# Performance work log

Measured on AMD Instinct MI355X. Metric: run time of the kernel, lower is better.

## Reference

```python
import jax, jax.numpy as jnp
import numpy as np

B, S, D, H = 4, 2048, 512, 16
HD = D // H          # head_dim = 32
ROPE_DIM = HD        # rope_pct = 1.0
NEG = -1e30


def apply_rope(x):
    # x: [B, H, S, HD]; rotate first ROPE_DIM dims, half-split (NeoX) convention
    half = ROPE_DIM // 2
    pos = jnp.arange(S, dtype=jnp.float32)
    inv_freq = 1.0 / (10000.0 ** (jnp.arange(0, ROPE_DIM, 2, dtype=jnp.float32) / ROPE_DIM))
    ang = pos[:, None] * inv_freq[None, :]          # [S, half]
    cos, sin = jnp.cos(ang), jnp.sin(ang)           # broadcast over B,H
    x1 = x[..., :half]
    x2 = x[..., half:ROPE_DIM]
    r1 = x1 * cos - x2 * sin
    r2 = x2 * cos + x1 * sin
    rest = x[..., ROPE_DIM:]
    return jnp.concatenate([r1, r2, rest], axis=-1)


def setup_inputs() -> dict:
    key = jax.random.key(0)
    ks = jax.random.split(key, 7)
    x = jax.random.normal(ks[0], (B, S, D), dtype=jnp.float32)
    # causal mask: True = block (j > i)
    attn_mask = jnp.triu(jnp.ones((S, S), dtype=bool), k=1)
    # padding mask: True = PAD; random lengths in [S//2, S]
    lengths = jax.random.randint(ks[1], (B,), S // 2, S + 1)
    key_padding_mask = jnp.arange(S)[None, :] >= lengths[:, None]
    scale = D ** -0.5
    Wq = jax.random.normal(ks[2], (D, D), dtype=jnp.float32) * scale
    Wk = jax.random.normal(ks[3], (D, D), dtype=jnp.float32) * scale
    Wv = jax.random.normal(ks[4], (D, D), dtype=jnp.float32) * scale
    Wo = jax.random.normal(ks[5], (D, D), dtype=jnp.float32) * scale
    return {"x": x, "attn_mask": attn_mask, "key_padding_mask": key_padding_mask,
            "Wq": Wq, "Wk": Wk, "Wv": Wv, "Wo": Wo}


def reference(x, attn_mask, key_padding_mask, Wq, Wk, Wv, Wo):
    scale = HD ** -0.5
    # nn.Linear: y = x @ W.T
    q = (x @ Wq.T).reshape(B, S, H, HD).transpose(0, 2, 1, 3)  # [B,H,S,HD]
    k = (x @ Wk.T).reshape(B, S, H, HD).transpose(0, 2, 1, 3)
    v = (x @ Wv.T).reshape(B, S, H, HD).transpose(0, 2, 1, 3)
    q = apply_rope(q)
    k = apply_rope(k)
    scores = jnp.einsum('bhid,bhjd->bhij', q, k) * scale       # [B,H,S,S]
    scores = jnp.where(key_padding_mask[:, None, None, :], NEG, scores)
    scores = jnp.where(attn_mask[None, None, :, :], NEG, scores)
    probs = jax.nn.softmax(scores.astype(jnp.float32), axis=-1)
    probs = jnp.nan_to_num(probs, nan=0.0)
    ctx = jnp.einsum('bhij,bhjd->bhid', probs, v)              # [B,H,S,HD]
    ctx = ctx.transpose(0, 2, 1, 3).reshape(B, S, D)
    ctx = jnp.where(key_padding_mask[:, :, None], 0.0, ctx)
    return ctx @ Wo.T
```

## Files before the change

kernel.cpp:

```cpp
#include <hip/hip_runtime.h>
#include <hip/hip_bf16.h>

#define B_ 4
#define S_ 2048
#define D_ 512
#define H_ 16
#define HD_ 32

typedef __bf16 bf16;
typedef __bf16 bf16x4 __attribute__((ext_vector_type(4)));
typedef __bf16 bf16x8 __attribute__((ext_vector_type(8)));
typedef float f32x4 __attribute__((ext_vector_type(4)));

__device__ __forceinline__ f32x4 mfma16(bf16x8 a, bf16x8 b, f32x4 c) {
  return __builtin_amdgcn_mfma_f32_16x16x32_bf16(a, b, c, 0, 0, 0);
}

__device__ __forceinline__ void gload16(const bf16* g, bf16* l) {
  __builtin_amdgcn_global_load_lds(
      (const __attribute__((address_space(1))) void*)g,
      (__attribute__((address_space(3))) void*)l, 16, 0, 0);
}

__device__ __forceinline__ bf16x8 cvt8(const float* __restrict__ p) {
  const f32x4* v = (const f32x4*)p;
  f32x4 a = v[0], b = v[1];
  bf16x8 r;
  r[0] = (bf16)a[0]; r[1] = (bf16)a[1]; r[2] = (bf16)a[2]; r[3] = (bf16)a[3];
  r[4] = (bf16)b[0]; r[5] = (bf16)b[1]; r[6] = (bf16)b[2]; r[7] = (bf16)b[3];
  return r;
}

__device__ __forceinline__ bf16x8 pack8(f32x4 a, f32x4 b) {
  bf16x8 r;
  r[0] = (bf16)a[0]; r[1] = (bf16)a[1]; r[2] = (bf16)a[2]; r[3] = (bf16)a[3];
  r[4] = (bf16)b[0]; r[5] = (bf16)b[1]; r[6] = (bf16)b[2]; r[7] = (bf16)b[3];
  return r;
}

__global__ __launch_bounds__(256) void prep_kernel(
    const float* __restrict__ wq, const float* __restrict__ wk,
    const float* __restrict__ wv, const float* __restrict__ wo,
    const unsigned char* __restrict__ am, const unsigned char* __restrict__ kpm,
    bf16* __restrict__ dq, bf16* __restrict__ dk, bf16* __restrict__ dv,
    bf16* __restrict__ dwo, int* __restrict__ lengths_out,
    float* __restrict__ costab, float* __restrict__ sintab) {
  int bid = blockIdx.x;
  if (bid < 512) {
    int mat = bid >> 7;
    size_t i = (size_t)(bid & 127) * 256 + threadIdx.x;
    const float* s = (mat == 0) ? wq : (mat == 1) ? wk : (mat == 2) ? wv : wo;
    bf16* d = (mat == 0) ? dq : (mat == 1) ? dk : (mat == 2) ? dv : dwo;
    *(bf16x8*)(d + i * 8) = cvt8(s + i * 8);
  } else if (bid == 512) {
    int b = threadIdx.x >> 6, lane = threadIdx.x & 63;
    int esize;
    if (am[1] == 1) esize = 1;
    else if (am[2] == 0x80 && am[3] == 0x3F) esize = 2;
    else if (am[3] == 0x3C) esize = 2;
    else if (am[4] == 1) esize = 4;
    else if (am[6] == 0x80 && am[7] == 0x3F) esize = 4;
    else if (am[8] == 1) esize = 8;
    else esize = 1;
    int cnt = 0;
    for (int i = lane; i < S_; i += 64) {
      size_t off = ((size_t)b * S_ + i) * (size_t)esize;
      unsigned char nz = 0;
      for (int e = 0; e < esize; ++e) nz |= kpm[off + e];
      cnt += (nz == 0) ? 1 : 0;
    }
    for (int off = 1; off < 64; off <<= 1) cnt += __shfl_xor(cnt, off);
    if (lane == 0) lengths_out[b] = cnt;
  } else {
    int ti = (bid - 513) * 256 + threadIdx.x;
    int s = ti >> 4, cc = ti & 15;
    float invf = powf(10000.0f, -(float)cc * (1.0f / 16.0f));
    float ang = (float)s * invf;
    costab[ti] = cosf(ang);
    sintab[ti] = sinf(ang);
  }
}

__global__ __launch_bounds__(256) void qkv_rope_kernel(
    const float* __restrict__ x, const bf16* __restrict__ Wq,
    const bf16* __restrict__ Wk, const bf16* __restrict__ Wv,
    const float* __restrict__ costab, const float* __restrict__ sintab,
    bf16* __restrict__ q_ws, bf16* __restrict__ k_ws, bf16* __restrict__ vt_ws) {
  __shared__ __align__(16) bf16 smem[12288];
#define AS(b) (smem + (b) * 2048)
#define BS(b) (smem + 4096 + (b) * 4096)
#define CT smem

  int bid = (blockIdx.x & 7) * 192 + (blockIdx.x >> 3);
  int brow = bid / 12, bc = bid % 12;
  int mat = bc >> 2;
  const bf16* W = (mat == 0) ? Wq : (mat == 1) ? Wk : Wv;
  int row0 = brow * 64;
  int col0 = (bc & 3) * 128;

  int tid = threadIdx.x;
  int w = tid >> 6, l = tid & 63;
  int wr = w >> 1, wc = w & 1;
  int g = l >> 4, c = l & 15;
  int lrow = l >> 2;
  int lcol = (l & 3) * 8;
  int arow = tid >> 2;
  int acol = (tid & 3) * 8;

  f32x4 acc[2][4];
  f32x4 zero = {0.f, 0.f, 0.f, 0.f};
#pragma unroll
  for (int m = 0; m < 2; ++m)
#pragma unroll
    for (int n = 0; n < 4; ++n) acc[m][n] = zero;

  *(bf16x8*)(AS(0) + arow * 32 + acol) =
      cvt8(x + (size_t)(row0 + arow) * 512 + acol);
#pragma unroll
  for (int j = 0; j < 2; ++j) {
    int chunk = w * 2 + j;
    gload16(W + (size_t)(col0 + chunk * 16 + lrow) * 512 + lcol,
            BS(0) + chunk * 512);
  }
  __syncthreads();
  int cur = 0;

#pragma unroll 1
  for (int k0 = 0; k0 < 512; k0 += 32) {
    bool more = (k0 < 480);
    f32x4 a0, a1;
    if (more) {
      const f32x4* src =
          (const f32x4*)(x + (size_t)(row0 + arow) * 512 + k0 + 32 + acol);
      a0 = src[0];
      a1 = src[1];
#pragma unroll
      for (int j = 0; j < 2; ++j) {
        int chunk = w * 2 + j;
        gload16(W + (size_t)(col0 + chunk * 16 + lrow) * 512 + k0 + 32 + lcol,
                BS(cur ^ 1) + chunk * 512);
      }
    }
    bf16x8 af[2], bfr[4];
#pragma unroll
    for (int m = 0; m < 2; ++m)
      af[m] = *(const bf16x8*)(AS(cur) + (wr * 32 + m * 16 + c) * 32 + g * 8);
#pragma unroll
    for (int n = 0; n < 4; ++n)
      bfr[n] = *(const bf16x8*)(BS(cur) + (wc * 64 + n * 16 + c) * 32 + g * 8);
#pragma unroll
    for (int m = 0; m < 2; ++m)
#pragma unroll
      for (int n = 0; n < 4; ++n) acc[m][n] = mfma16(af[m], bfr[n], acc[m][n]);
    if (more) {
      *(bf16x8*)(AS(cur ^ 1) + arow * 32 + acol) = pack8(a0, a1);
      __syncthreads();
      cur ^= 1;
    }
  }

  if (mat < 2) {
    bf16* dst = (mat == 0) ? q_ws : k_ws;
    const float esc =
        (mat == 0) ? (0.17677669529663687f * 1.4426950408889634f) : 1.0f;
#pragma unroll
    for (int m = 0; m < 2; ++m) {
      int rbase = row0 + wr * 32 + m * 16 + g * 4;
#pragma unroll
      for (int r = 0; r < 4; ++r) {
        int grow = rbase + r;
        int bb = grow >> 11, s = grow & (S_ - 1);
        float cs = costab[s * 16 + c];
        float sn = sintab[s * 16 + c];
#pragma unroll
        for (int np = 0; np < 2; ++np) {
          int n = np * 2;
          int obase = col0 + wc * 64 + n * 16;
          int h = obase >> 5;
          float a0v = acc[m][n][r], a1v = acc[m][n + 1][r];
          size_t base = (((size_t)bb * H_ + h) * S_ + s) * HD_;
          dst[base + c] = (bf16)((a0v * cs - a1v * sn) * esc);
          dst[base + c + 16] = (bf16)((a1v * cs + a0v * sn) * esc);
        }
      }
    }
  } else {
    __syncthreads();
#pragma unroll
    for (int m = 0; m < 2; ++m) {
#pragma unroll
      for (int n = 0; n < 4; ++n) {
        int o = wc * 64 + n * 16 + c;
        int sb = wr * 32 + m * 16 + g * 4;
        bf16x4 q4;
        q4[0] = (bf16)acc[m][n][0]; q4[1] = (bf16)acc[m][n][1];
        q4[2] = (bf16)acc[m][n][2]; q4[3] = (bf16)acc[m][n][3];
        *(bf16x4*)(&CT[o * 72 + sb]) = q4;
      }
    }
    __syncthreads();
    int o_l = tid >> 1, sh = (tid & 1) * 32;
    int o = col0 + o_l;
    int h = o >> 5, hd = o & 31;
    int bb2 = row0 >> 11, sr = row0 & (S_ - 1);
    size_t dst = (((size_t)bb2 * H_ + h) * HD_ + hd) * S_ + sr + sh;
#pragma unroll
    for (int j = 0; j < 4; ++j)
      *(bf16x8*)(vt_ws + dst + j * 8) =
          *(const bf16x8*)(&CT[o_l * 72 + sh + j * 8]);
  }
#undef AS
#undef BS
#undef CT
}

__global__ __launch_bounds__(256) void attn_kernel(
    const bf16* __restrict__ q_ws, const bf16* __restrict__ k_ws,
    const bf16* __restrict__ vt_ws, const int* __restrict__ lengths,
    bf16* __restrict__ ctx_ws) {
  __shared__ __align__(16) bf16 Ks[2][4096];
  __shared__ __align__(16) bf16 Vts[2][4096];
  __shared__ __align__(16) bf16 Ps[4][1024];

  int id = blockIdx.x;
  int xcd = id & 7;
  int ix = id >> 3;
  int p = ix & 15;
  int bh = xcd + 8 * (ix >> 4);
  int bb = bh >> 4, h = bh & 15;
  int tid = threadIdx.x, w = tid >> 6, l = tid & 63, g = l >> 4, c = l & 15;
  const size_t bh_base = ((size_t)bb * H_ + h) * (size_t)S_ * HD_;
  int len = lengths[bb];
  int rowrel = w * 16 + c;

  int srowK = w * 16 + (l & 15), skgK = l >> 4;
  int srowV = w * 8 + (l & 7), ssgV = l >> 3;
  int slotK8 = (skgK * 16 + (srowK & 15) + ((srowK >> 4) << 6)) * 8;
  int slotV8 =
      ((ssgV & 3) * 16 + (srowV & 15) + (((ssgV >> 2) + ((srowV >> 4) << 1)) << 6)) * 8;

  bf16 one = (bf16)1.0f;
  bf16x8 onesf;
#pragma unroll
  for (int i = 0; i < 8; ++i) onesf[i] = one;

#pragma unroll 1
  for (int phase = 0; phase < 2; ++phase) {
    int qt = phase ? (31 - p) : p;
    int q0 = qt * 64 + w * 16;
    int T = qt + 1;

    bf16x8 qf = *(const bf16x8*)(q_ws + bh_base + (size_t)(q0 + c) * HD_ + g * 8);

    f32x4 zero = {0.f, 0.f, 0.f, 0.f};
    f32x4 ctxa[2];
    ctxa[0] = zero; ctxa[1] = zero;
    f32x4 lsum = zero;

    const bf16* kbase = k_ws + bh_base + (size_t)srowK * HD_ + skgK * 8;
    const bf16* vbase = vt_ws + bh_base + (size_t)srowV * S_ + ssgV * 8;

    bf16x8 rK0 = *(const bf16x8*)kbase;
    bf16x8 rV0 = *(const bf16x8*)vbase;
    bf16x8 rK1 = rK0, rV1 = rV0;
    if (T > 1) {
      rK1 = *(const bf16x8*)(kbase + 64 * HD_);
      rV1 = *(const bf16x8*)(vbase + 64);
    }
    __syncthreads();
    *(bf16x8*)(&Ks[0][slotK8]) = rK0;
    *(bf16x8*)(&Vts[0][slotV8]) = rV0;
    *(bf16x8*)(&Ks[0][2048 + slotK8]) = rK1;
    *(bf16x8*)(&Vts[0][2048 + slotV8]) = rV1;
    __syncthreads();
    int cur = 0;

    auto body = [&](int t, int off) {
      const bf16* KsC = &Ks[cur][off];
      const bf16* VtsC = &Vts[cur][off];
      f32x4 sacc[4];
#pragma unroll
      for (int n = 0; n < 4; ++n) {
        bf16x8 kf = *(const bf16x8*)(&KsC[(l + (n << 6)) * 8]);
        sacc[n] = mfma16(kf, qf, zero);
      }

      float sv[4][4];
      if (t != qt) {
#pragma unroll
        for (int n = 0; n < 4; ++n)
#pragma unroll
          for (int r = 0; r < 4; ++r)
            sv[n][r] = __builtin_amdgcn_exp2f(sacc[n][r]);
      } else {
#pragma unroll
        for (int n = 0; n < 4; ++n) {
          int jr = n * 16 + g * 4;
#pragma unroll
          for (int r = 0; r < 4; ++r) {
            float e = __builtin_amdgcn_exp2f(sacc[n][r]);
            sv[n][r] = (jr + r > rowrel) ? 0.f : e;
          }
        }
      }

#pragma unroll
      for (int n = 0; n < 4; ++n) {
        bf16x4 pk;
        pk[0] = (bf16)sv[n][0]; pk[1] = (bf16)sv[n][1];
        pk[2] = (bf16)sv[n][2]; pk[3] = (bf16)sv[n][3];
        int chunk = 2 * n + (g >> 1);
        int poff = ((chunk >> 2) << 9) + ((chunk & 3) * 16 + c) * 8 + ((g & 1) << 2);
        *(bf16x4*)(&Ps[w][poff]) = pk;
      }

      bf16x8 pf0 = *(const bf16x8*)(&Ps[w][l * 8]);
      bf16x8 pf1 = *(const bf16x8*)(&Ps[w][512 + l * 8]);

      lsum = mfma16(pf0, onesf, lsum);
      lsum = mfma16(pf1, onesf, lsum);

#pragma unroll
      for (int n2 = 0; n2 < 2; ++n2) {
        bf16x8 v0 = *(const bf16x8*)(&VtsC[(l + ((2 * n2) << 6)) * 8]);
        bf16x8 v1 = *(const bf16x8*)(&VtsC[(l + ((1 + 2 * n2) << 6)) * 8]);
        ctxa[n2] = mfma16(pf0, v0, ctxa[n2]);
        ctxa[n2] = mfma16(pf1, v1, ctxa[n2]);
      }
    };

#pragma unroll 1
    for (int r = 0;; ++r) {
      int t0 = 2 * r, t1 = 2 * r + 1;
      bool more = (t0 + 2 < T);
      if (more) {
        const bf16* kp = kbase + (size_t)(t0 + 2) * 64 * HD_;
        const bf16* vp = vbase + (t0 + 2) * 64;
        rK0 = *(const bf16x8*)kp;
        rV0 = *(const bf16x8*)vp;
        rK1 = *(const bf16x8*)(kp + 64 * HD_);
        rV1 = *(const bf16x8*)(vp + 64);
      }
      body(t0, 0);
      if (t1 < T) body(t1, 2048);
      if (!more) break;
      *(bf16x8*)(&Ks[cur ^ 1][slotK8]) = rK0;
      *(bf16x8*)(&Vts[cur ^ 1][slotV8]) = rV0;
      *(bf16x8*)(&Ks[cur ^ 1][2048 + slotK8]) = rK1;
      *(bf16x8*)(&Vts[cur ^ 1][2048 + slotV8]) = rV1;
      __syncthreads();
      cur ^= 1;
    }

#pragma unroll
    for (int n = 0; n < 2; ++n)
#pragma unroll
      for (int r = 0; r < 4; ++r) {
        int qr = q0 + g * 4 + r;
        float val = ctxa[n][r] / lsum[r];
        if (qr >= len) val = 0.f;
        ctx_ws[(((size_t)bb * S_ + qr) * H_ + h) * HD_ + n * 16 + c] = (bf16)val;
      }
  }
}

__global__ __launch_bounds__(256) void out_proj_kernel(
    const bf16* __restrict__ ctx, const bf16* __restrict__ Wo,
    float* __restrict__ out) {
  __shared__ __align__(16) bf16 As[2][2048];
  __shared__ __align__(16) bf16 Bs[2][4096];

  int bid = (blockIdx.x & 7) * 64 + (blockIdx.x >> 3);
  int brow = bid >> 2, bc = bid & 3;
  int row0 = brow * 64, col0 = bc * 128;
  int tid = threadIdx.x;
  int w = tid >> 6, l = tid & 63;
  int wr = w >> 1, wc = w & 1;
  int g = l >> 4, c = l & 15;
  int lrow = l >> 2;
  int lcol = (l & 3) * 8;

  f32x4 acc[2][4];
  f32x4 zero = {0.f, 0.f, 0.f, 0.f};
#pragma unroll
  for (int m = 0; m < 2; ++m)
#pragma unroll
    for (int n = 0; n < 4; ++n) acc[m][n] = zero;

#pragma unroll
  for (int j = 0; j < 3; ++j) {
    int chunk = w * 3 + j;
    if (chunk < 4)
      gload16(ctx + (size_t)(row0 + chunk * 16 + lrow) * 512 + lcol,
              As[0] + chunk * 512);
    else
      gload16(Wo + (size_t)(col0 + (chunk - 4) * 16 + lrow) * 512 + lcol,
              Bs[0] + (chunk - 4) * 512);
  }
  __syncthreads();
  int cur = 0;

#pragma unroll 1
  for (int k0 = 0; k0 < 512; k0 += 32) {
    bool more = (k0 < 480);
    if (more) {
#pragma unroll
      for (int j = 0; j < 3; ++j) {
        int chunk = w * 3 + j;
        if (chunk < 4)
          gload16(ctx + (size_t)(row0 + chunk * 16 + lrow) * 512 + k0 + 32 + lcol,
                  As[cur ^ 1] + chunk * 512);
        else
          gload16(Wo + (size_t)(col0 + (chunk - 4) * 16 + lrow) * 512 + k0 + 32 +
                      lcol,
                  Bs[cur ^ 1] + (chunk - 4) * 512);
      }
    }
    bf16x8 af[2], bfr[4];
#pragma unroll
    for (int m = 0; m < 2; ++m)
      af[m] = *(const bf16x8*)(As[cur] + (wr * 32 + m * 16 + c) * 32 + g * 8);
#pragma unroll
    for (int n = 0; n < 4; ++n)
      bfr[n] = *(const bf16x8*)(Bs[cur] + (wc * 64 + n * 16 + c) * 32 + g * 8);
#pragma unroll
    for (int m = 0; m < 2; ++m)
#pragma unroll
      for (int n = 0; n < 4; ++n) acc[m][n] = mfma16(af[m], bfr[n], acc[m][n]);
    if (more) {
      __syncthreads();
      cur ^= 1;
    }
  }

#pragma unroll
  for (int m = 0; m < 2; ++m) {
    int rbase = row0 + wr * 32 + m * 16 + g * 4;
#pragma unroll
    for (int n = 0; n < 4; ++n) {
      int o = col0 + wc * 64 + n * 16 + c;
#pragma unroll
      for (int r = 0; r < 4; ++r)
        out[(size_t)(rbase + r) * 512 + o] = acc[m][n][r];
    }
  }
}

extern "C" void kernel_launch(void* const* d_in, const int* in_sizes, int n_in,
                              void* d_out, int out_size, void* d_ws,
                              size_t ws_size, hipStream_t stream) {
  const float* x = (const float*)d_in[0];
  const unsigned char* am = (const unsigned char*)d_in[1];
  const unsigned char* kpm = (const unsigned char*)d_in[2];
  const float* Wq = (const float*)d_in[3];
  const float* Wk = (const float*)d_in[4];
  const float* Wv = (const float*)d_in[5];
  const float* Wo = (const float*)d_in[6];
  float* out = (float*)d_out;

  char* ws = (char*)d_ws;
  int* lengths = (int*)ws;
  const size_t QKV_ELEMS = (size_t)B_ * H_ * S_ * HD_;
  const size_t W_ELEMS = (size_t)D_ * D_;
  bf16* ctx_ws = (bf16*)(ws + 256);
  bf16* q_ws = ctx_ws + QKV_ELEMS;
  bf16* k_ws = q_ws + QKV_ELEMS;
  bf16* vt_ws = k_ws + QKV_ELEMS;
  bf16* wqb = vt_ws + QKV_ELEMS;
  bf16* wkb = wqb + W_ELEMS;
  bf16* wvb = wkb + W_ELEMS;
  bf16* wob = wvb + W_ELEMS;
  float* costab = (float*)(wob + W_ELEMS);
  float* sintab = costab + (size_t)S_ * 16;

  hipLaunchKernelGGL(prep_kernel, dim3(641), dim3(256), 0, stream, Wq, Wk, Wv,
                     Wo, am, kpm, wqb, wkb, wvb, wob, lengths, costab, sintab);
  hipLaunchKernelGGL(qkv_rope_kernel, dim3(1536), dim3(256), 0, stream, x, wqb,
                     wkb, wvb, costab, sintab, q_ws, k_ws, vt_ws);
  hipLaunchKernelGGL(attn_kernel, dim3(1024), dim3(256), 0, stream, q_ws, k_ws,
                     vt_ws, lengths, ctx_ws);
  hipLaunchKernelGGL(out_proj_kernel, dim3(512), dim3(256), 0, stream, ctx_ws,
                     wob, out);
}
```

Measured before the change: 109.0 us.

## Process paired causal query tiles in one pass sharing K/V tile loads

The two query tiles p and 31-p, previously handled in sequential phases each streaming its own causal K/V range, are now processed together in a single loop over the longer range. Each staged K/V tile is read once from LDS and reused by both query tiles, with tile A skipped past its causal limit. This removes the redundant global and LDS loading of the shared K/V prefix and one phase's setup and synchronisation. In exchange it doubles the accumulator and fragment registers per thread, which may lower occupancy.

```diff
diff --git a/kernel.cpp b/kernel.cpp
--- a/kernel.cpp
+++ b/kernel.cpp
@@ -233,6 +233,10 @@
   int len = lengths[bb];
   int rowrel = w * 16 + c;
 
+  int qtA = p, qtB = 31 - p;
+  int Tu = 32 - p;
+  int q0A = qtA * 64 + w * 16, q0B = qtB * 64 + w * 16;
+
   int srowK = w * 16 + (l & 15), skgK = l >> 4;
   int srowV = w * 8 + (l & 7), ssgV = l >> 3;
   int slotK8 = (skgK * 16 + (srowK & 15) + ((srowK >> 4) << 6)) * 8;
@@ -244,124 +248,133 @@
 #pragma unroll
   for (int i = 0; i < 8; ++i) onesf[i] = one;
 
-#pragma unroll 1
-  for (int phase = 0; phase < 2; ++phase) {
-    int qt = phase ? (31 - p) : p;
-    int q0 = qt * 64 + w * 16;
-    int T = qt + 1;
-
-    bf16x8 qf = *(const bf16x8*)(q_ws + bh_base + (size_t)(q0 + c) * HD_ + g * 8);
-
-    f32x4 zero = {0.f, 0.f, 0.f, 0.f};
-    f32x4 ctxa[2];
-    ctxa[0] = zero; ctxa[1] = zero;
-    f32x4 lsum = zero;
-
-    const bf16* kbase = k_ws + bh_base + (size_t)srowK * HD_ + skgK * 8;
-    const bf16* vbase = vt_ws + bh_base + (size_t)srowV * S_ + ssgV * 8;
-
-    bf16x8 rK0 = *(const bf16x8*)kbase;
-    bf16x8 rV0 = *(const bf16x8*)vbase;
-    bf16x8 rK1 = rK0, rV1 = rV0;
-    if (T > 1) {
-      rK1 = *(const bf16x8*)(kbase + 64 * HD_);
-      rV1 = *(const bf16x8*)(vbase + 64);
-    }
-    __syncthreads();
-    *(bf16x8*)(&Ks[0][slotK8]) = rK0;
-    *(bf16x8*)(&Vts[0][slotV8]) = rV0;
-    *(bf16x8*)(&Ks[0][2048 + slotK8]) = rK1;
-    *(bf16x8*)(&Vts[0][2048 + slotV8]) = rV1;
-    __syncthreads();
-    int cur = 0;
-
-    auto body = [&](int t, int off) {
-      const bf16* KsC = &Ks[cur][off];
-      const bf16* VtsC = &Vts[cur][off];
-      f32x4 sacc[4];
+  bf16x8 qfA =
+      *(const bf16x8*)(q_ws + bh_base + (size_t)(q0A + c) * HD_ + g * 8);
+  bf16x8 qfB =
+      *(const bf16x8*)(q_ws + bh_base + (size_t)(q0B + c) * HD_ + g * 8);
+
+  f32x4 zero = {0.f, 0.f, 0.f, 0.f};
+  f32x4 ctxaA[2], ctxaB[2];
+  ctxaA[0] = zero; ctxaA[1] = zero;
+  ctxaB[0] = zero; ctxaB[1] = zero;
+  f32x4 lsumA = zero, lsumB = zero;
+
+  const bf16* kbase = k_ws + bh_base + (size_t)srowK * HD_ + skgK * 8;
+  const bf16* vbase = vt_ws + bh_base + (size_t)srowV * S_ + ssgV * 8;
+
+  bf16x8 rK0 = *(const bf16x8*)kbase;
+  bf16x8 rV0 = *(const bf16x8*)vbase;
+  bf16x8 rK1 = *(const bf16x8*)(kbase + 64 * HD_);
+  bf16x8 rV1 = *(const bf16x8*)(vbase + 64);
+  *(bf16x8*)(&Ks[0][slotK8]) = rK0;
+  *(bf16x8*)(&Vts[0][slotV8]) = rV0;
+  *(bf16x8*)(&Ks[0][2048 + slotK8]) = rK1;
+  *(bf16x8*)(&Vts[0][2048 + slotV8]) = rV1;
+  __syncthreads();
+  int cur = 0;
+
+  auto body = [&](int qt, const bf16x8& qf, f32x4* ctxa, f32x4& lsum, int t,
+                  const bf16x8(&kf)[4], const bf16x8(&vf)[4]) {
+    f32x4 sacc[4];
+#pragma unroll
+    for (int n = 0; n < 4; ++n) sacc[n] = mfma16(kf[n], qf, zero);
+
+    float sv[4][4];
+    if (t != qt) {
+#pragma unroll
+      for (int n = 0; n < 4; ++n)
+#pragma unroll
+        for (int r = 0; r < 4; ++r)
+          sv[n][r] = __builtin_amdgcn_exp2f(sacc[n][r]);
+    } else {
 #pragma unroll
       for (int n = 0; n < 4; ++n) {
-        bf16x8 kf = *(const bf16x8*)(&KsC[(l + (n << 6)) * 8]);
-        sacc[n] = mfma16(kf, qf, zero);
-      }
-
-      float sv[4][4];
-      if (t != qt) {
-#pragma unroll
-        for (int n = 0; n < 4; ++n)
-#pragma unroll
-          for (int r = 0; r < 4; ++r)
-            sv[n][r] = __builtin_amdgcn_exp2f(sacc[n][r]);
-      } else {
-#pragma unroll
-        for (int n = 0; n < 4; ++n) {
-          int jr = n * 16 + g * 4;
-#pragma unroll
-          for (int r = 0; r < 4; ++r) {
-            float e = __builtin_amdgcn_exp2f(sacc[n][r]);
-            sv[n][r] = (jr + r > rowrel) ? 0.f : e;
-          }
+        int jr = n * 16 + g * 4;
+#pragma unroll
+        for (int r = 0; r < 4; ++r) {
+          float e = __builtin_amdgcn_exp2f(sacc[n][r]);
+          sv[n][r] = (jr + r > rowrel) ? 0.f : e;
         }
       }
-
-#pragma unroll
-      for (int n = 0; n < 4; ++n) {
-        bf16x4 pk;
-        pk[0] = (bf16)sv[n][0]; pk[1] = (bf16)sv[n][1];
-        pk[2] = (bf16)sv[n][2]; pk[3] = (bf16)sv[n][3];
-        int chunk = 2 * n + (g >> 1);
-        int poff = ((chunk >> 2) << 9) + ((chunk & 3) * 16 + c) * 8 + ((g & 1) << 2);
-        *(bf16x4*)(&Ps[w][poff]) = pk;
-      }
-
-      bf16x8 pf0 = *(const bf16x8*)(&Ps[w][l * 8]);
-      bf16x8 pf1 = *(const bf16x8*)(&Ps[w][512 + l * 8]);
-
-      lsum = mfma16(pf0, onesf, lsum);
-      lsum = mfma16(pf1, onesf, lsum);
-
-#pragma unroll
-      for (int n2 = 0; n2 < 2; ++n2) {
-        bf16x8 v0 = *(const bf16x8*)(&VtsC[(l + ((2 * n2) << 6)) * 8]);
-        bf16x8 v1 = *(const bf16x8*)(&VtsC[(l + ((1 + 2 * n2) << 6)) * 8]);
-        ctxa[n2] = mfma16(pf0, v0, ctxa[n2]);
-        ctxa[n2] = mfma16(pf1, v1, ctxa[n2]);
-      }
-    };
+    }
+
+#pragma unroll
+    for (int n = 0; n < 4; ++n) {
+      bf16x4 pk;
+      pk[0] = (bf16)sv[n][0]; pk[1] = (bf16)sv[n][1];
+      pk[2] = (bf16)sv[n][2]; pk[3] = (bf16)sv[n][3];
+      int chunk = 2 * n + (g >> 1);
+      int poff = ((chunk >> 2) << 9) + ((chunk & 3) * 16 + c) * 8 + ((g & 1) << 2);
+      *(bf16x4*)(&Ps[w][poff]) = pk;
+    }
+
+    bf16x8 pf0 = *(const bf16x8*)(&Ps[w][l * 8]);
+    bf16x8 pf1 = *(const bf16x8*)(&Ps[w][512 + l * 8]);
+
+    lsum = mfma16(pf0, onesf, lsum);
+    lsum = mfma16(pf1, onesf, lsum);
+
+#pragma unroll
+    for (int n2 = 0; n2 < 2; ++n2) {
+      ctxa[n2] = mfma16(pf0, vf[2 * n2], ctxa[n2]);
+      ctxa[n2] = mfma16(pf1, vf[2 * n2 + 1], ctxa[n2]);
+    }
+  };
+
+  auto tile = [&](int t, int off) {
+    const bf16* KsC = &Ks[cur][off];
+    const bf16* VtsC = &Vts[cur][off];
+    bf16x8 kf[4], vf[4];
+#pragma unroll
+    for (int k = 0; k < 4; ++k) {
+      kf[k] = *(const bf16x8*)(&KsC[(l + (k << 6)) * 8]);
+      vf[k] = *(const bf16x8*)(&VtsC[(l + (k << 6)) * 8]);
+    }
+    if (t <= qtA) body(qtA, qfA, ctxaA, lsumA, t, kf, vf);
+    body(qtB, qfB, ctxaB, lsumB, t, kf, vf);
+  };
 
 #pragma unroll 1
-    for (int r = 0;; ++r) {
-      int t0 = 2 * r, t1 = 2 * r + 1;
-      bool more = (t0 + 2 < T);
-      if (more) {
-        const bf16* kp = kbase + (size_t)(t0 + 2) * 64 * HD_;
-        const bf16* vp = vbase + (t0 + 2) * 64;
-        rK0 = *(const bf16x8*)kp;
-        rV0 = *(const bf16x8*)vp;
-        rK1 = *(const bf16x8*)(kp + 64 * HD_);
-        rV1 = *(const bf16x8*)(vp + 64);
-      }
-      body(t0, 0);
-      if (t1 < T) body(t1, 2048);
-      if (!more) break;
-      *(bf16x8*)(&Ks[cur ^ 1][slotK8]) = rK0;
-      *(bf16x8*)(&Vts[cur ^ 1][slotV8]) = rV0;
-      *(bf16x8*)(&Ks[cur ^ 1][2048 + slotK8]) = rK1;
-      *(bf16x8*)(&Vts[cur ^ 1][2048 + slotV8]) = rV1;
-      __syncthreads();
-      cur ^= 1;
-    }
-
-#pragma unroll
-    for (int n = 0; n < 2; ++n)
-#pragma unroll
-      for (int r = 0; r < 4; ++r) {
-        int qr = q0 + g * 4 + r;
-        float val = ctxa[n][r] / lsum[r];
-        if (qr >= len) val = 0.f;
-        ctx_ws[(((size_t)bb * S_ + qr) * H_ + h) * HD_ + n * 16 + c] = (bf16)val;
-      }
-  }
+  for (int r = 0;; ++r) {
+    int t0 = 2 * r, t1 = t0 + 1;
+    bool more = (t0 + 2 < Tu);
+    if (more) {
+      const bf16* kp = kbase + (size_t)(t0 + 2) * 64 * HD_;
+      const bf16* vp = vbase + (t0 + 2) * 64;
+      rK0 = *(const bf16x8*)kp;
+      rV0 = *(const bf16x8*)vp;
+      rK1 = *(const bf16x8*)(kp + 64 * HD_);
+      rV1 = *(const bf16x8*)(vp + 64);
+    }
+    tile(t0, 0);
+    if (t1 < Tu) tile(t1, 2048);
+    if (!more) break;
+    *(bf16x8*)(&Ks[cur ^ 1][slotK8]) = rK0;
+    *(bf16x8*)(&Vts[cur ^ 1][slotV8]) = rV0;
+    *(bf16x8*)(&Ks[cur ^ 1][2048 + slotK8]) = rK1;
+    *(bf16x8*)(&Vts[cur ^ 1][2048 + slotV8]) = rV1;
+    __syncthreads();
+    cur ^= 1;
+  }
+
+#pragma unroll
+  for (int n = 0; n < 2; ++n)
+#pragma unroll
+    for (int r = 0; r < 4; ++r) {
+      int qr = q0A + g * 4 + r;
+      float val = ctxaA[n][r] / lsumA[r];
+      if (qr >= len) val = 0.f;
+      ctx_ws[(((size_t)bb * S_ + qr) * H_ + h) * HD_ + n * 16 + c] = (bf16)val;
+    }
+#pragma unroll
+  for (int n = 0; n < 2; ++n)
+#pragma unroll
+    for (int r = 0; r < 4; ++r) {
+      int qr = q0B + g * 4 + r;
+      float val = ctxaB[n][r] / lsumB[r];
+      if (qr >= len) val = 0.f;
+      ctx_ws[(((size_t)bb * S_ + qr) * H_ + h) * HD_ + n * 16 + c] = (bf16)val;
+    }
 }
 
 __global__ __launch_bounds__(256) void out_proj_kernel(
```

Result: slower. 114.8 us (+5.3%).
